# Kernel optimization log

Hardware: AMD Instinct MI355X
Metric: run time of the kernel (lower is better)

## Reference

```python
import jax, jax.numpy as jnp
import numpy as np

EMBED_DIM = 1024
NUM_HEADS = 16
HEAD_DIM = EMBED_DIM // NUM_HEADS
FF_DIM = 4 * EMBED_DIM
LN_EPS = 1e-5


def _layernorm(x, g, b):
    mu = jnp.mean(x, axis=-1, keepdims=True)
    var = jnp.var(x, axis=-1, keepdims=True)
    return (x - mu) * jax.lax.rsqrt(var + LN_EPS) * g + b


def setup_inputs() -> dict:
    key = jax.random.key(0)
    ks = jax.random.split(key, 8)
    B, T, C = 2, 2048, EMBED_DIM
    s_c = 1.0 / np.sqrt(C)
    s_f = 1.0 / np.sqrt(FF_DIM)
    return {
        "x": jax.random.normal(ks[0], (B, T, C), jnp.float32),
        "ln1_g": jnp.ones((C,), jnp.float32),
        "ln1_b": jnp.zeros((C,), jnp.float32),
        "qkv_w": jax.random.uniform(ks[1], (C, 3 * C), jnp.float32, -s_c, s_c),
        "qkv_b": jnp.zeros((3 * C,), jnp.float32),
        "out_w": jax.random.uniform(ks[2], (C, C), jnp.float32, -s_c, s_c),
        "out_b": jnp.zeros((C,), jnp.float32),
        "ln2_g": jnp.ones((C,), jnp.float32),
        "ln2_b": jnp.zeros((C,), jnp.float32),
        "ff1_w": jax.random.uniform(ks[3], (C, FF_DIM), jnp.float32, -s_c, s_c),
        "ff1_b": jnp.zeros((FF_DIM,), jnp.float32),
        "ff2_w": jax.random.uniform(ks[4], (FF_DIM, C), jnp.float32, -s_f, s_f),
        "ff2_b": jnp.zeros((C,), jnp.float32),
    }


def reference(x, ln1_g, ln1_b, qkv_w, qkv_b, out_w, out_b,
              ln2_g, ln2_b, ff1_w, ff1_b, ff2_w, ff2_b):
    B, T, C = x.shape
    H, D = NUM_HEADS, HEAD_DIM

    # --- pre-LN causal self-attention ---
    h = _layernorm(x, ln1_g, ln1_b)
    qkv = h @ qkv_w + qkv_b                      # [B,T,3C]
    q, k, v = jnp.split(qkv, 3, axis=-1)
    q = q.reshape(B, T, H, D)
    k = k.reshape(B, T, H, D)
    v = v.reshape(B, T, H, D)
    scores = jnp.einsum('bqhd,bkhd->bhqk', q, k) / np.sqrt(D)  # [B,H,T,T]
    causal = jnp.tril(jnp.ones((T, T), bool))
    scores = jnp.where(causal, scores, -jnp.inf)
    attn = jax.nn.softmax(scores, axis=-1)
    o = jnp.einsum('bhqk,bkhd->bqhd', attn, v).reshape(B, T, C)
    x = x + o @ out_w + out_b

    # --- GELU MLP ---
    h2 = _layernorm(x, ln2_g, ln2_b)
    ff = jax.nn.gelu(h2 @ ff1_w + ff1_b, approximate=False) @ ff2_w + ff2_b
    return x + ff
```

## Files before the change

### kernel.cpp

```cpp
#include <hip/hip_runtime.h>
#include <hip/hip_bf16.h>
#include <math.h>

#define B_ 2
#define T_ 2048
#define C_ 1024
#define H_ 16
#define D_ 64
#define F_ 4096
#define BT_ (B_*T_)

typedef __attribute__((ext_vector_type(8))) short bf16x8;
typedef __attribute__((ext_vector_type(4))) float f32x4;

__device__ __forceinline__ float bfraw2f(unsigned int u){
    union { unsigned int i; float f; } c; c.i = u << 16; return c.f;
}
__device__ __forceinline__ short f2bfraw(float f){
    union { float f; unsigned int i; } c; c.f = f;
    unsigned int u = c.i;
    u += 0x7fffu + ((u >> 16) & 1u);
    return (short)(u >> 16);
}
__device__ __forceinline__ void gl2lds16(const void* g, void* l) {
    __builtin_amdgcn_global_load_lds(
        (const __attribute__((address_space(1))) unsigned int*)g,
        (__attribute__((address_space(3))) unsigned int*)l,
        16, 0, 0);
}

__global__ __launch_bounds__(256) void wconv_t(const float* __restrict__ W,
                                               short* __restrict__ Wt,
                                               int K, int N)
{
    __shared__ short tile[64][65];
    int k0 = blockIdx.y * 64, n0 = blockIdx.x * 64;
    int t = threadIdx.x;
#pragma unroll
    for (int i = 0; i < 4; i++) {
        int idx = t + i * 256;
        int r = idx >> 4, c4 = (idx & 15) * 4;
        float4 u = *(const float4*)(W + (size_t)(k0 + r) * N + n0 + c4);
        tile[c4 + 0][r] = f2bfraw(u.x);
        tile[c4 + 1][r] = f2bfraw(u.y);
        tile[c4 + 2][r] = f2bfraw(u.z);
        tile[c4 + 3][r] = f2bfraw(u.w);
    }
    __syncthreads();
#pragma unroll
    for (int i = 0; i < 2; i++) {
        int idx = t + i * 256;
        int r = idx >> 3, c8 = (idx & 7) * 8;
        short v[8];
#pragma unroll
        for (int u8 = 0; u8 < 8; u8++) v[u8] = tile[r][c8 + u8];
        *(uint4*)(Wt + (size_t)(n0 + r) * K + k0 + c8) = *(const uint4*)v;
    }
}

__global__ __launch_bounds__(256) void v_transpose(const __hip_bfloat16* __restrict__ qkv,
                                                   short* __restrict__ vt)
{
    __shared__ short tile[64][65];
    int kb = blockIdx.x * 64;
    int h = blockIdx.y, b = blockIdx.z;
    const short* src = (const short*)qkv + (size_t)b * T_ * 3 * C_ + 2 * C_ + h * D_;
    int t = threadIdx.x;
#pragma unroll
    for (int i = 0; i < 2; i++) {
        int idx = t + i * 256;
        int r = idx >> 3, c8 = (idx & 7) * 8;
        bf16x8 v = *(const bf16x8*)(src + (size_t)(kb + r) * 3 * C_ + c8);
#pragma unroll
        for (int u = 0; u < 8; u++) tile[c8 + u][r] = v[u];
    }
    __syncthreads();
    short* dst = vt + (size_t)(b * H_ + h) * D_ * T_ + kb;
#pragma unroll
    for (int i = 0; i < 2; i++) {
        int idx = t + i * 256;
        int r = idx >> 3, c8 = (idx & 7) * 8;
        short v[8];
#pragma unroll
        for (int u = 0; u < 8; u++) v[u] = tile[r][c8 + u];
        *(uint4*)(dst + (size_t)r * T_ + c8) = *(const uint4*)v;
    }
}

__global__ __launch_bounds__(256) void ln_fused(const float* __restrict__ x, int ldx,
                                                const float* __restrict__ g,
                                                const float* __restrict__ b,
                                                __hip_bfloat16* out, int ldo)
{
    __shared__ float sm1[4], sm2[4];
    __shared__ float smu, srs;
    int row = blockIdx.x, t = threadIdx.x;
    const float* xr = x + (size_t)row * ldx;
    float v[4]; float s = 0.f, ss = 0.f;
#pragma unroll
    for (int i = 0; i < 4; i++) {
        float f = xr[t + i * 256];
        v[i] = f; s += f; ss += f * f;
    }
#pragma unroll
    for (int off = 32; off >= 1; off >>= 1) {
        s  += __shfl_xor(s,  off);
        ss += __shfl_xor(ss, off);
    }
    int wave = t >> 6, lane = t & 63;
    if (!lane) { sm1[wave] = s; sm2[wave] = ss; }
    __syncthreads();
    if (t == 0) {
        s  = sm1[0] + sm1[1] + sm1[2] + sm1[3];
        ss = sm2[0] + sm2[1] + sm2[2] + sm2[3];
        float mu  = s * (1.f / C_);
        float var = ss * (1.f / C_) - mu * mu;
        if (var < 0.f) var = 0.f;
        smu = mu; srs = rsqrtf(var + 1e-5f);
    }
    __syncthreads();
    float mu = smu, rs = srs;
#pragma unroll
    for (int i = 0; i < 4; i++) {
        int c = t + i * 256;
        out[(size_t)row * ldo + c] = __float2bfloat16((v[i] - mu) * rs * g[c] + b[c]);
    }
}

template<int ACT>
__global__ __launch_bounds__(256) void gemm128(
    const __hip_bfloat16* A, int lda,
    const short* Wt, int ldw, int noff, int koff,
    const float* __restrict__ bias, int boff,
    void* out, int ldo,
    int K)
{
    __shared__ __align__(16) short As[128 * 32];
    __shared__ __align__(16) short Bs[128 * 32];
    int tid = threadIdx.x;
    int w = tid >> 6, lane = tid & 63;
    int quad = lane >> 4, l16 = lane & 15;
    int wm = w >> 1, wn = w & 1;
    int m0 = blockIdx.y * 128, n0 = blockIdx.x * 128;
    int lr = lane >> 2, lk = (lane & 3) * 8;

    const __hip_bfloat16* Ag = A + (size_t)(m0 + w * 32 + lr) * lda + lk;
    const short*          Bg = Wt + (size_t)(noff + n0 + w * 32 + lr) * ldw + koff + lk;
    short* Al0 = &As[(w * 32) * 32];
    short* Al1 = &As[(w * 32 + 16) * 32];
    short* Bl0 = &Bs[(w * 32) * 32];
    short* Bl1 = &Bs[(w * 32 + 16) * 32];

    f32x4 acc[4][4];
#pragma unroll
    for (int i = 0; i < 4; i++)
#pragma unroll
        for (int j = 0; j < 4; j++) acc[i][j] = (f32x4){0.f, 0.f, 0.f, 0.f};

    for (int k0 = 0; k0 < K; k0 += 32) {
        gl2lds16(Ag + k0,            Al0);
        gl2lds16(Ag + 16 * lda + k0, Al1);
        gl2lds16(Bg + k0,            Bl0);
        gl2lds16(Bg + 16 * ldw + k0, Bl1);
        __syncthreads();
        bf16x8 af[4], bfr[4];
#pragma unroll
        for (int mt = 0; mt < 4; mt++)
            af[mt] = *(const bf16x8*)&As[(wm * 64 + mt * 16 + l16) * 32 + quad * 8];
#pragma unroll
        for (int nt = 0; nt < 4; nt++)
            bfr[nt] = *(const bf16x8*)&Bs[(wn * 64 + nt * 16 + l16) * 32 + quad * 8];
#pragma unroll
        for (int mt = 0; mt < 4; mt++)
#pragma unroll
            for (int nt = 0; nt < 4; nt++)
                acc[mt][nt] = __builtin_amdgcn_mfma_f32_16x16x32_bf16(af[mt], bfr[nt], acc[mt][nt], 0, 0, 0);
        __syncthreads();
    }

#pragma unroll
    for (int nt = 0; nt < 4; nt++) {
        int c = n0 + wn * 64 + nt * 16 + l16;
        float bv = bias ? bias[boff + c] : 0.f;
#pragma unroll
        for (int mt = 0; mt < 4; mt++) {
#pragma unroll
            for (int reg = 0; reg < 4; reg++) {
                int r = m0 + wm * 64 + mt * 16 + quad * 4 + reg;
                float v = acc[mt][nt][reg] + bv;
                if (ACT == 1) v = 0.5f * v * (1.f + erff(v * 0.70710678118654752f));
                ((__hip_bfloat16*)out)[(size_t)r * ldo + c] = __float2bfloat16(v);
            }
        }
    }
}

__global__ __launch_bounds__(256) void gemm64(
    const __hip_bfloat16* A, int lda,
    const short* Wt, int ldw, int koff,
    const float* __restrict__ bias,
    const float* res, int ldres,
    float* out, int ldo,
    int K)
{
    __shared__ __align__(16) short As[64 * 32];
    __shared__ __align__(16) short Bs[128 * 32];
    int tid = threadIdx.x;
    int w = tid >> 6, lane = tid & 63;
    int quad = lane >> 4, l16 = lane & 15;
    int m0 = blockIdx.y * 64, n0 = blockIdx.x * 128;
    int lr = lane >> 2, lk = (lane & 3) * 8;

    const __hip_bfloat16* Ag = A + (size_t)(m0 + w * 16 + lr) * lda + lk;
    const short*          Bg = Wt + (size_t)(n0 + w * 32 + lr) * ldw + koff + lk;
    short* Al  = &As[(w * 16) * 32];
    short* Bl0 = &Bs[(w * 32) * 32];
    short* Bl1 = &Bs[(w * 32 + 16) * 32];

    f32x4 acc[8];
#pragma unroll
    for (int j = 0; j < 8; j++) acc[j] = (f32x4){0.f, 0.f, 0.f, 0.f};

    for (int k0 = 0; k0 < K; k0 += 32) {
        gl2lds16(Ag + k0,            Al);
        gl2lds16(Bg + k0,            Bl0);
        gl2lds16(Bg + 16 * ldw + k0, Bl1);
        __syncthreads();
        bf16x8 af = *(const bf16x8*)&As[(w * 16 + l16) * 32 + quad * 8];
#pragma unroll
        for (int nt = 0; nt < 8; nt++) {
            bf16x8 bfr = *(const bf16x8*)&Bs[(nt * 16 + l16) * 32 + quad * 8];
            acc[nt] = __builtin_amdgcn_mfma_f32_16x16x32_bf16(af, bfr, acc[nt], 0, 0, 0);
        }
        __syncthreads();
    }

#pragma unroll
    for (int nt = 0; nt < 8; nt++) {
        int c = n0 + nt * 16 + l16;
        float bv = bias ? bias[c] : 0.f;
#pragma unroll
        for (int reg = 0; reg < 4; reg++) {
            int r = m0 + w * 16 + quad * 4 + reg;
            float v = acc[nt][reg] + bv + res[(size_t)r * ldres + c];
            out[(size_t)r * ldo + c] = v;
        }
    }
}

__global__ __launch_bounds__(256, 2) void attn_flash(__hip_bfloat16* qkv,
                                                     const short* __restrict__ vt)
{
    __shared__ __align__(16) short Ks[2][64 * 64];
    __shared__ __align__(16) short Vs[2][64 * 64];
    __shared__ __align__(16) short Pl[4][16 * 72];
    int tid = threadIdx.x;
    int wave = tid >> 6, lane = tid & 63;
    int quad = lane >> 4, l16 = lane & 15;
    int fid = blockIdx.x + 16 * blockIdx.y;
    int h = (fid & 7) * 2 + ((fid >> 3) >> 4);
    int i = (fid >> 3) & 15;
    int b = blockIdx.z;
    int qbs[2]; qbs[0] = i; qbs[1] = 31 - i;
    const size_t rs = 3 * C_;
    __hip_bfloat16* base = qkv + (size_t)b * T_ * rs;
    const __hip_bfloat16* Qb = base + h * D_;
    const __hip_bfloat16* Kb = base + C_ + h * D_;
    const short* Vt = vt + (size_t)(b * H_ + h) * D_ * T_;

    bf16x8 qf[2][2];
#pragma unroll
    for (int tq = 0; tq < 2; tq++) {
        const __hip_bfloat16* qr = Qb + (size_t)(qbs[tq] * 64 + wave * 16 + l16) * rs + quad * 8;
        qf[tq][0] = *(const bf16x8*)qr;
        qf[tq][1] = *(const bf16x8*)(qr + 32);
    }

    f32x4 o[2][4];
    float m[2][4], l[2][4];
#pragma unroll
    for (int tq = 0; tq < 2; tq++)
#pragma unroll
        for (int t = 0; t < 4; t++) {
            o[tq][t] = (f32x4){0.f, 0.f, 0.f, 0.f};
            m[tq][t] = -INFINITY;
            l[tq][t] = 0.f;
        }
    short* Pw = &Pl[wave][0];

    int srow = wave * 16 + (lane >> 3);
    int scg  = ((lane & 7) ^ (lane >> 3)) * 8;
    const __hip_bfloat16* Kg = Kb + (size_t)srow * rs + scg;
    const short*          Vg = Vt + (size_t)srow * T_ + scg;

    int cur = 0;
#pragma unroll
    for (int j = 0; j < 2; j++) {
        gl2lds16(Kg + (size_t)(j * 8) * rs, &Ks[0][(wave * 2 + j) * 512]);
        gl2lds16(Vg + (size_t)(j * 8) * T_, &Vs[0][(wave * 2 + j) * 512]);
    }
    __syncthreads();

    int qhi = qbs[1];
    int swz = (l16 & 7);
    for (int kt = 0; kt <= qhi; kt++) {
        if (kt < qhi) {
            int kb = (kt + 1) * 64;
#pragma unroll
            for (int j = 0; j < 2; j++) {
                gl2lds16(Kg + (size_t)(kb + j * 8) * rs, &Ks[cur ^ 1][(wave * 2 + j) * 512]);
                gl2lds16(Vg + (size_t)(j * 8) * T_ + kb, &Vs[cur ^ 1][(wave * 2 + j) * 512]);
            }
        }
        const short* Kc = Ks[cur];
        const short* Vc = Vs[cur];
#pragma unroll
        for (int tq = 0; tq < 2; tq++) {
            if (tq == 0 && kt > qbs[0]) continue;
            f32x4 sa[4];
            __builtin_amdgcn_s_setprio(1);
#pragma unroll
            for (int t16 = 0; t16 < 4; t16++) {
                int row = t16 * 16 + l16;
                bf16x8 kf0 = *(const bf16x8*)&Kc[row * 64 + ((quad     ^ swz)) * 8];
                bf16x8 kf1 = *(const bf16x8*)&Kc[row * 64 + (((quad + 4) ^ swz)) * 8];
                f32x4 s = (f32x4){0.f, 0.f, 0.f, 0.f};
                s = __builtin_amdgcn_mfma_f32_16x16x32_bf16(qf[tq][0], kf0, s, 0, 0, 0);
                s = __builtin_amdgcn_mfma_f32_16x16x32_bf16(qf[tq][1], kf1, s, 0, 0, 0);
                sa[t16] = s;
            }
            __builtin_amdgcn_s_setprio(0);
            bool maskit = (kt == qbs[tq]);
#pragma unroll
            for (int t16 = 0; t16 < 4; t16++) {
#pragma unroll
                for (int reg = 0; reg < 4; reg++) {
                    float v = sa[t16][reg] * 0.125f;
                    if (maskit) {
                        int keyl = t16 * 16 + l16;
                        int ql = wave * 16 + quad * 4 + reg;
                        if (keyl > ql) v = -3.0e38f;
                    }
                    sa[t16][reg] = v;
                }
            }
            float mx[4];
#pragma unroll
            for (int reg = 0; reg < 4; reg++)
                mx[reg] = fmaxf(fmaxf(sa[0][reg], sa[1][reg]), fmaxf(sa[2][reg], sa[3][reg]));
#pragma unroll
            for (int off = 8; off >= 1; off >>= 1)
#pragma unroll
                for (int reg = 0; reg < 4; reg++)
                    mx[reg] = fmaxf(mx[reg], __shfl_xor(mx[reg], off));
            float alpha[4];
#pragma unroll
            for (int reg = 0; reg < 4; reg++) {
                float mn = fmaxf(m[tq][reg], mx[reg]);
                alpha[reg] = __expf(m[tq][reg] - mn);
                m[tq][reg] = mn;
            }
            float rsum[4] = {0.f, 0.f, 0.f, 0.f};
#pragma unroll
            for (int t16 = 0; t16 < 4; t16++) {
#pragma unroll
                for (int reg = 0; reg < 4; reg++) {
                    float p = __expf(sa[t16][reg] - m[tq][reg]);
                    rsum[reg] += p;
                    Pw[(quad * 4 + reg) * 72 + t16 * 16 + l16] = f2bfraw(p);
                }
            }
#pragma unroll
            for (int off = 8; off >= 1; off >>= 1)
#pragma unroll
                for (int reg = 0; reg < 4; reg++)
                    rsum[reg] += __shfl_xor(rsum[reg], off);
#pragma unroll
            for (int reg = 0; reg < 4; reg++)
                l[tq][reg] = l[tq][reg] * alpha[reg] + rsum[reg];
#pragma unroll
            for (int t = 0; t < 4; t++)
#pragma unroll
                for (int reg = 0; reg < 4; reg++)
                    o[tq][t][reg] *= alpha[reg];
            __builtin_amdgcn_s_setprio(1);
#pragma unroll
            for (int chunk = 0; chunk < 2; chunk++) {
                bf16x8 pf = *(const bf16x8*)&Pw[l16 * 72 + chunk * 32 + quad * 8];
#pragma unroll
                for (int dt = 0; dt < 4; dt++) {
                    int row = dt * 16 + l16;
                    bf16x8 vf = *(const bf16x8*)&Vc[row * 64 + (((chunk * 4 + quad) ^ swz)) * 8];
                    o[tq][dt] = __builtin_amdgcn_mfma_f32_16x16x32_bf16(pf, vf, o[tq][dt], 0, 0, 0);
                }
            }
            __builtin_amdgcn_s_setprio(0);
        }
        __syncthreads();
        cur ^= 1;
    }

#pragma unroll
    for (int tq = 0; tq < 2; tq++) {
#pragma unroll
        for (int dt = 0; dt < 4; dt++) {
#pragma unroll
            for (int reg = 0; reg < 4; reg++) {
                int r = qbs[tq] * 64 + wave * 16 + quad * 4 + reg;
                float v = o[tq][dt][reg] / l[tq][reg];
                base[(size_t)r * rs + h * D_ + dt * 16 + l16] = __float2bfloat16(v);
            }
        }
    }
}

extern "C" void kernel_launch(void* const* d_in, const int* in_sizes, int n_in,
                              void* d_out, int out_size, void* d_ws, size_t ws_size,
                              hipStream_t stream)
{
    const float* x     = (const float*)d_in[0];
    const float* ln1_g = (const float*)d_in[1];
    const float* ln1_b = (const float*)d_in[2];
    const float* qkv_w = (const float*)d_in[3];
    const float* qkv_b = (const float*)d_in[4];
    const float* out_w = (const float*)d_in[5];
    const float* out_b = (const float*)d_in[6];
    const float* ln2_g = (const float*)d_in[7];
    const float* ln2_b = (const float*)d_in[8];
    const float* ff1_w = (const float*)d_in[9];
    const float* ff1_b = (const float*)d_in[10];
    const float* ff2_w = (const float*)d_in[11];
    const float* ff2_b = (const float*)d_in[12];

    char* ws = (char*)d_ws;
    __hip_bfloat16* qkv = (__hip_bfloat16*)ws;
    short* qkvwT = (short*)(ws + 25165824);
    short* outwT = (short*)(ws + 31457280);
    short* ff1wT = (short*)(ws + 33554432);
    short* ff2wT = (short*)(ws + 41943040);
    __hip_bfloat16* hbuf2 = qkv;
    __hip_bfloat16* act   = qkv + 1024;
    __hip_bfloat16* hbuf1 = (__hip_bfloat16*)d_out;
    float* x1 = (float*)d_out;
    short* vtbuf = (short*)d_out;

    wconv_t<<<dim3(3 * C_ / 64, C_ / 64), 256, 0, stream>>>(qkv_w, qkvwT, C_, 3 * C_);
    wconv_t<<<dim3(C_ / 64, C_ / 64),     256, 0, stream>>>(out_w, outwT, C_, C_);
    wconv_t<<<dim3(F_ / 64, C_ / 64),     256, 0, stream>>>(ff1_w, ff1wT, C_, F_);
    wconv_t<<<dim3(C_ / 64, F_ / 64),     256, 0, stream>>>(ff2_w, ff2wT, F_, C_);

    ln_fused<<<BT_, 256, 0, stream>>>(x, C_, ln1_g, ln1_b, hbuf1, C_);
    gemm128<0><<<dim3(3 * C_ / 128, BT_ / 128), 256, 0, stream>>>(
        hbuf1, C_, qkvwT, C_, 0, 0, qkv_b, 0, qkv, 3 * C_, C_);
    v_transpose<<<dim3(T_ / 64, H_, B_), 256, 0, stream>>>(qkv, vtbuf);
    attn_flash<<<dim3(16, H_, B_), 256, 0, stream>>>(qkv, vtbuf);
    gemm64<<<dim3(C_ / 128, BT_ / 64), 256, 0, stream>>>(
        qkv, 3 * C_, outwT, C_, 0, out_b, x, C_, x1, C_, C_);
    ln_fused<<<BT_, 256, 0, stream>>>(x1, C_, ln2_g, ln2_b, hbuf2, 3 * C_);
    for (int f = 0; f < 2; f++) {
        gemm128<1><<<dim3(2048 / 128, BT_ / 128), 256, 0, stream>>>(
            hbuf2, 3 * C_, ff1wT, C_, f * 2048, 0, ff1_b, f * 2048,
            act, 3 * C_, C_);
        gemm64<<<dim3(C_ / 128, BT_ / 64), 256, 0, stream>>>(
            act, 3 * C_, ff2wT, F_, f * 2048, (f == 0 ? ff2_b : nullptr),
            x1, C_, x1, C_, 2048);
    }
}
```

Measured before the change: 441.2 us.

## Retile residual GEMM to 128x64 with 2x2 waves; skip rare softmax rescales

The residual-add GEMM changes from a 64x128 tile with each wave owning 16 rows to a 128x64 tile with a 2x2 wave grid, each wave computing a 64x32 sub-tile. Each wave now loads 4 A and 2 B fragments per k-step for 8 MFMAs, instead of 1 A and 8 B fragments, so register-level reuse rises and LDS reads per MFMA fall. In flash attention, the running-max update and rescaling of l and o are skipped when no lane's new block max exceeds the stored max by more than 8. This lazy-rescale trick removes exp and multiply work on most iterations, at the cost of a wave-wide vote and exponentials that may reach up to e^8 before normalisation.

```diff
diff --git a/kernel.cpp b/kernel.cpp
--- a/kernel.cpp
+++ b/kernel.cpp
@@ -195,7 +195,7 @@
     }
 }
 
-__global__ __launch_bounds__(256) void gemm64(
+__global__ __launch_bounds__(256) void gemm64n(
     const __hip_bfloat16* A, int lda,
     const short* Wt, int ldw, int koff,
     const float* __restrict__ bias,
@@ -203,47 +203,59 @@
     float* out, int ldo,
     int K)
 {
-    __shared__ __align__(16) short As[64 * 32];
-    __shared__ __align__(16) short Bs[128 * 32];
+    __shared__ __align__(16) short As[128 * 32];
+    __shared__ __align__(16) short Bs[64 * 32];
     int tid = threadIdx.x;
     int w = tid >> 6, lane = tid & 63;
     int quad = lane >> 4, l16 = lane & 15;
-    int m0 = blockIdx.y * 64, n0 = blockIdx.x * 128;
+    int wm = w >> 1, wn = w & 1;
+    int m0 = blockIdx.y * 128, n0 = blockIdx.x * 64;
     int lr = lane >> 2, lk = (lane & 3) * 8;
 
-    const __hip_bfloat16* Ag = A + (size_t)(m0 + w * 16 + lr) * lda + lk;
-    const short*          Bg = Wt + (size_t)(n0 + w * 32 + lr) * ldw + koff + lk;
-    short* Al  = &As[(w * 16) * 32];
-    short* Bl0 = &Bs[(w * 32) * 32];
-    short* Bl1 = &Bs[(w * 32 + 16) * 32];
-
-    f32x4 acc[8];
-#pragma unroll
-    for (int j = 0; j < 8; j++) acc[j] = (f32x4){0.f, 0.f, 0.f, 0.f};
+    const __hip_bfloat16* Ag = A + (size_t)(m0 + w * 32 + lr) * lda + lk;
+    const short*          Bg = Wt + (size_t)(n0 + w * 16 + lr) * ldw + koff + lk;
+    short* Al0 = &As[(w * 32) * 32];
+    short* Al1 = &As[(w * 32 + 16) * 32];
+    short* Bl  = &Bs[(w * 16) * 32];
+
+    f32x4 acc[4][2];
+#pragma unroll
+    for (int i = 0; i < 4; i++)
+#pragma unroll
+        for (int j = 0; j < 2; j++) acc[i][j] = (f32x4){0.f, 0.f, 0.f, 0.f};
 
     for (int k0 = 0; k0 < K; k0 += 32) {
-        gl2lds16(Ag + k0,            Al);
-        gl2lds16(Bg + k0,            Bl0);
-        gl2lds16(Bg + 16 * ldw + k0, Bl1);
+        gl2lds16(Ag + k0,            Al0);
+        gl2lds16(Ag + 16 * lda + k0, Al1);
+        gl2lds16(Bg + k0,            Bl);
         __syncthreads();
-        bf16x8 af = *(const bf16x8*)&As[(w * 16 + l16) * 32 + quad * 8];
-#pragma unroll
-        for (int nt = 0; nt < 8; nt++) {
-            bf16x8 bfr = *(const bf16x8*)&Bs[(nt * 16 + l16) * 32 + quad * 8];
-            acc[nt] = __builtin_amdgcn_mfma_f32_16x16x32_bf16(af, bfr, acc[nt], 0, 0, 0);
-        }
+        bf16x8 af[4], bfr[2];
+#pragma unroll
+        for (int mt = 0; mt < 4; mt++)
+            af[mt] = *(const bf16x8*)&As[(wm * 64 + mt * 16 + l16) * 32 + quad * 8];
+#pragma unroll
+        for (int nt = 0; nt < 2; nt++)
+            bfr[nt] = *(const bf16x8*)&Bs[(wn * 32 + nt * 16 + l16) * 32 + quad * 8];
+#pragma unroll
+        for (int mt = 0; mt < 4; mt++)
+#pragma unroll
+            for (int nt = 0; nt < 2; nt++)
+                acc[mt][nt] = __builtin_amdgcn_mfma_f32_16x16x32_bf16(af[mt], bfr[nt], acc[mt][nt], 0, 0, 0);
         __syncthreads();
     }
 
 #pragma unroll
-    for (int nt = 0; nt < 8; nt++) {
-        int c = n0 + nt * 16 + l16;
+    for (int nt = 0; nt < 2; nt++) {
+        int c = n0 + wn * 32 + nt * 16 + l16;
         float bv = bias ? bias[c] : 0.f;
 #pragma unroll
-        for (int reg = 0; reg < 4; reg++) {
-            int r = m0 + w * 16 + quad * 4 + reg;
-            float v = acc[nt][reg] + bv + res[(size_t)r * ldres + c];
-            out[(size_t)r * ldo + c] = v;
+        for (int mt = 0; mt < 4; mt++) {
+#pragma unroll
+            for (int reg = 0; reg < 4; reg++) {
+                int r = m0 + wm * 64 + mt * 16 + quad * 4 + reg;
+                float v = acc[mt][nt][reg] + bv + res[(size_t)r * ldres + c];
+                out[(size_t)r * ldo + c] = v;
+            }
         }
     }
 }
@@ -353,12 +365,22 @@
 #pragma unroll
                 for (int reg = 0; reg < 4; reg++)
                     mx[reg] = fmaxf(mx[reg], __shfl_xor(mx[reg], off));
-            float alpha[4];
-#pragma unroll
-            for (int reg = 0; reg < 4; reg++) {
-                float mn = fmaxf(m[tq][reg], mx[reg]);
-                alpha[reg] = __expf(m[tq][reg] - mn);
-                m[tq][reg] = mn;
+            bool small = (mx[0] <= m[tq][0] + 8.f) & (mx[1] <= m[tq][1] + 8.f)
+                       & (mx[2] <= m[tq][2] + 8.f) & (mx[3] <= m[tq][3] + 8.f);
+            if (!__all(small)) {
+                float alpha[4];
+#pragma unroll
+                for (int reg = 0; reg < 4; reg++) {
+                    float mn = fmaxf(m[tq][reg], mx[reg]);
+                    alpha[reg] = __expf(m[tq][reg] - mn);
+                    m[tq][reg] = mn;
+                    l[tq][reg] *= alpha[reg];
+                }
+#pragma unroll
+                for (int t = 0; t < 4; t++)
+#pragma unroll
+                    for (int reg = 0; reg < 4; reg++)
+                        o[tq][t][reg] *= alpha[reg];
             }
             float rsum[4] = {0.f, 0.f, 0.f, 0.f};
 #pragma unroll
@@ -377,12 +399,7 @@
                     rsum[reg] += __shfl_xor(rsum[reg], off);
 #pragma unroll
             for (int reg = 0; reg < 4; reg++)
-                l[tq][reg] = l[tq][reg] * alpha[reg] + rsum[reg];
-#pragma unroll
-            for (int t = 0; t < 4; t++)
-#pragma unroll
-                for (int reg = 0; reg < 4; reg++)
-                    o[tq][t][reg] *= alpha[reg];
+                l[tq][reg] += rsum[reg];
             __builtin_amdgcn_s_setprio(1);
 #pragma unroll
             for (int chunk = 0; chunk < 2; chunk++) {
@@ -454,14 +471,14 @@
         hbuf1, C_, qkvwT, C_, 0, 0, qkv_b, 0, qkv, 3 * C_, C_);
     v_transpose<<<dim3(T_ / 64, H_, B_), 256, 0, stream>>>(qkv, vtbuf);
     attn_flash<<<dim3(16, H_, B_), 256, 0, stream>>>(qkv, vtbuf);
-    gemm64<<<dim3(C_ / 128, BT_ / 64), 256, 0, stream>>>(
+    gemm64n<<<dim3(C_ / 64, BT_ / 128), 256, 0, stream>>>(
         qkv, 3 * C_, outwT, C_, 0, out_b, x, C_, x1, C_, C_);
     ln_fused<<<BT_, 256, 0, stream>>>(x1, C_, ln2_g, ln2_b, hbuf2, 3 * C_);
     for (int f = 0; f < 2; f++) {
         gemm128<1><<<dim3(2048 / 128, BT_ / 128), 256, 0, stream>>>(
             hbuf2, 3 * C_, ff1wT, C_, f * 2048, 0, ff1_b, f * 2048,
             act, 3 * C_, C_);
-        gemm64<<<dim3(C_ / 128, BT_ / 64), 256, 0, stream>>>(
+        gemm64n<<<dim3(C_ / 64, BT_ / 128), 256, 0, stream>>>(
             act, 3 * C_, ff2wT, F_, f * 2048, (f == 0 ? ff2_b : nullptr),
             x1, C_, x1, C_, 2048);
     }
```

Measured after the change: 437.2 us. Within noise of the previous version (-0.9%).
